# Optimization experiments

Hardware: AMD Instinct MI355X
Metric: run time of the kernel (lower is better)

The kernel has to match this reference:

```python
import jax, jax.numpy as jnp
import numpy as np

NEG_SLOPE = 0.2   # PyG GATConv default negative_slope
LN_EPS = 1e-5
SOFTMAX_EPS = 1e-16  # PyG softmax denominator eps


def setup_inputs() -> dict:
    key = jax.random.key(0)
    ks = jax.random.split(key, 6)
    N, IN, OUT, H, E = 100000, 128, 64, 2, 1600000
    X = jax.random.normal(ks[0], (N, IN), dtype=jnp.float32)
    edge_index = jax.random.randint(ks[1], (2, E), 0, N, dtype=jnp.int64)
    W = jax.random.normal(ks[2], (H * OUT, IN), dtype=jnp.float32) * 0.05
    att_src = jax.random.normal(ks[3], (H, OUT), dtype=jnp.float32) * 0.05
    att_dst = jax.random.normal(ks[4], (H, OUT), dtype=jnp.float32) * 0.05
    bias = jnp.zeros((OUT,), dtype=jnp.float32)
    ln_gamma = jnp.ones((OUT,), dtype=jnp.float32)
    ln_beta = jnp.zeros((OUT,), dtype=jnp.float32)
    return {"X": X, "edge_index": edge_index, "W": W, "att_src": att_src,
            "att_dst": att_dst, "bias": bias, "ln_gamma": ln_gamma, "ln_beta": ln_beta}


def reference(X, edge_index, W, att_src, att_dst, bias, ln_gamma, ln_beta):
    N = X.shape[0]
    H, F = att_src.shape
    # PyG GATConv default: add self-loops
    loops = jnp.arange(N, dtype=edge_index.dtype)
    src = jnp.concatenate([edge_index[0], loops])  # [Et]
    dst = jnp.concatenate([edge_index[1], loops])  # [Et]
    # linear projection: x' = X @ W^T  -> [N, H, F]
    x = (X @ W.T).reshape(N, H, F)
    # per-node attention logits  [N, H]
    a_src = jnp.einsum('nhf,hf->nh', x, att_src)
    a_dst = jnp.einsum('nhf,hf->nh', x, att_dst)
    # per-edge logits, leaky relu  [Et, H]
    e = jax.nn.leaky_relu(a_src[src] + a_dst[dst], NEG_SLOPE)
    # segment softmax over incoming edges of each dst node
    m = jax.ops.segment_max(e, dst, num_segments=N)          # [N, H]
    ex = jnp.exp(e - m[dst])
    denom = jax.ops.segment_sum(ex, dst, num_segments=N)     # [N, H]
    alpha = ex / (denom[dst] + SOFTMAX_EPS)                  # [Et, H]
    # weighted scatter-add of source features
    msg = x[src] * alpha[:, :, None]                         # [Et, H, F]
    out = jax.ops.segment_sum(msg, dst, num_segments=N)      # [N, H, F]
    # concat=False -> mean over heads, then bias
    out = out.mean(axis=1) + bias                            # [N, F]
    # LayerNorm over features
    mu = out.mean(axis=-1, keepdims=True)
    var = ((out - mu) ** 2).mean(axis=-1, keepdims=True)
    h = (out - mu) * jax.lax.rsqrt(var + LN_EPS) * ln_gamma + ln_beta
    return h
```

## Files before the change

### kernel.cpp

```cpp
#include <hip/hip_runtime.h>
#include <hip/hip_bf16.h>

#define NEG_SLOPE 0.2f
#define LN_EPS 1e-5f
#define SM_EPS 1e-16f

typedef __attribute__((ext_vector_type(8))) short bf16x8;
typedef __attribute__((ext_vector_type(4))) float f32x4;

__device__ inline unsigned short f2bf(float f) {
    unsigned u = __float_as_uint(f);
    return (unsigned short)((u + 0x7FFFu + ((u >> 16) & 1u)) >> 16);
}
__device__ inline float bf_lo(unsigned int v) { return __uint_as_float(v << 16); }
__device__ inline float bf_hi(unsigned int v) { return __uint_as_float(v & 0xffff0000u); }

#define NBIN 512
#define BCAP 4864
#define SCHUNK 2048
#define CURPAD 16

__global__ __launch_bounds__(256) void k_gemm(const float* __restrict__ X,
                                              const float* __restrict__ W,
                                              const float* __restrict__ att_src,
                                              const float* __restrict__ att_dst,
                                              unsigned int* __restrict__ xp,
                                              float2* __restrict__ aS,
                                              float2* __restrict__ aD,
                                              int* __restrict__ binCursor, int N) {
    __shared__ unsigned short Ws[128 * 136];
    __shared__ unsigned short Xs[64 * 136];
    const int t = threadIdx.x;
    const int b0 = blockIdx.x * 64;
    const int lane = t & 63;
    const int w = t >> 6;
    const int c15 = lane & 15;
    const int quad = lane >> 4;

    if (blockIdx.x == 0) {
        for (int i = t; i < NBIN; i += 256) binCursor[i * CURPAD] = i * BCAP;
    }

#pragma unroll
    for (int i = 0; i < 16; ++i) {
        int f = i * 256 + t;
        int nr = f >> 5;
        int q = f & 31;
        float4 v = reinterpret_cast<const float4*>(W)[nr * 32 + q];
        ushort4 b;
        b.x = f2bf(v.x); b.y = f2bf(v.y); b.z = f2bf(v.z); b.w = f2bf(v.w);
        *reinterpret_cast<ushort4*>(&Ws[nr * 136 + q * 4]) = b;
    }
#pragma unroll
    for (int i = 0; i < 8; ++i) {
        int f = i * 256 + t;
        int m = f >> 5;
        int q = f & 31;
        int gr = b0 + m;
        if (gr >= N) gr = N - 1;
        float4 v = reinterpret_cast<const float4*>(X)[(size_t)gr * 32 + q];
        ushort4 b;
        b.x = f2bf(v.x); b.y = f2bf(v.y); b.z = f2bf(v.z); b.w = f2bf(v.w);
        *reinterpret_cast<ushort4*>(&Xs[m * 136 + q * 4]) = b;
    }
    __syncthreads();

    f32x4 acc[8];
#pragma unroll
    for (int ct = 0; ct < 8; ++ct) acc[ct] = (f32x4){0.f, 0.f, 0.f, 0.f};

#pragma unroll
    for (int kc = 0; kc < 4; ++kc) {
        bf16x8 af = *reinterpret_cast<const bf16x8*>(
            &Xs[(w * 16 + c15) * 136 + kc * 32 + quad * 8]);
#pragma unroll
        for (int ct = 0; ct < 8; ++ct) {
            bf16x8 bfr = *reinterpret_cast<const bf16x8*>(
                &Ws[(ct * 16 + c15) * 136 + kc * 32 + quad * 8]);
            acc[ct] = __builtin_amdgcn_mfma_f32_16x16x32_bf16(af, bfr, acc[ct], 0, 0, 0);
        }
    }

    float attS[8], attD[8];
#pragma unroll
    for (int ct = 0; ct < 8; ++ct) {
        attS[ct] = att_src[ct * 16 + c15];
        attD[ct] = att_dst[ct * 16 + c15];
    }

#pragma unroll
    for (int r = 0; r < 4; ++r) {
        int row = b0 + w * 16 + quad * 4 + r;
        float s0 = 0.f, s1 = 0.f, d0 = 0.f, d1 = 0.f;
#pragma unroll
        for (int ct = 0; ct < 4; ++ct) {
            s0 += acc[ct][r] * attS[ct];
            d0 += acc[ct][r] * attD[ct];
            s1 += acc[ct + 4][r] * attS[ct + 4];
            d1 += acc[ct + 4][r] * attD[ct + 4];
        }
#pragma unroll
        for (int o = 1; o < 16; o <<= 1) {
            s0 += __shfl_xor(s0, o);
            s1 += __shfl_xor(s1, o);
            d0 += __shfl_xor(d0, o);
            d1 += __shfl_xor(d1, o);
        }
        if (row < N) {
#pragma unroll
            for (int ct = 0; ct < 4; ++ct) {
                unsigned int p = (unsigned int)f2bf(acc[ct][r]) |
                                 ((unsigned int)f2bf(acc[ct + 4][r]) << 16);
                xp[(size_t)row * 64 + ct * 16 + c15] = p;
            }
            if (c15 == 0) {
                aS[row] = make_float2(s0, s1);
                aD[row] = make_float2(d0, d1);
            }
        }
    }
}

__global__ __launch_bounds__(256) void k_scatter(const int* __restrict__ ei,
                                                 const float2* __restrict__ aS,
                                                 const float2* __restrict__ aD,
                                                 int* __restrict__ binCursor,
                                                 uint2* __restrict__ tmp, int E) {
    __shared__ int off[NBIN];
    const int t = threadIdx.x;
    const int base = blockIdx.x * SCHUNK;

    int se[8], de[8];
    unsigned int ue[8];
#pragma unroll
    for (int k = 0; k < 8; ++k) {
        int i = base + k * 256 + t;
        if (i < E) {
            int s = ei[i];
            int d = ei[E + i];
            se[k] = s; de[k] = d;
            float2 a = aS[s];
            float2 ad2 = aD[d];
            float f0 = a.x + ad2.x; f0 = fmaxf(f0, NEG_SLOPE * f0);
            float f1 = a.y + ad2.y; f1 = fmaxf(f1, NEG_SLOPE * f1);
            ue[k] = (unsigned int)f2bf(__expf(f0)) |
                    ((unsigned int)f2bf(__expf(f1)) << 16);
        } else {
            de[k] = -1;
        }
    }

    for (int i = t; i < NBIN; i += 256) off[i] = 0;
    __syncthreads();
#pragma unroll
    for (int k = 0; k < 8; ++k)
        if (de[k] >= 0) atomicAdd(&off[de[k] >> 8], 1);
    __syncthreads();
    for (int i = t; i < NBIN; i += 256) {
        int h = off[i];
        off[i] = h ? atomicAdd(&binCursor[i * CURPAD], h) : 0;
    }
    __syncthreads();
#pragma unroll
    for (int k = 0; k < 8; ++k) {
        if (de[k] >= 0) {
            int p = atomicAdd(&off[de[k] >> 8], 1);
            tmp[p] = make_uint2(((unsigned)(de[k] & 255) << 24) | (unsigned)se[k],
                                ue[k]);
        }
    }
}

__global__ __launch_bounds__(512) void k_bucket(const uint2* __restrict__ tmp,
                                                const int* __restrict__ binCursor,
                                                uint2* __restrict__ csr,
                                                unsigned int* __restrict__ rowPtr,
                                                int N) {
    __shared__ int cnt[256];
    __shared__ int cur[256];
    __shared__ int lds[4];
    const int t = threadIdx.x;
    const int b = blockIdx.x;
    const int start = b * BCAP;
    int m = binCursor[b * CURPAD] - start;
    if (m > BCAP) m = BCAP;

    if (t < 256) cnt[t] = 0;
    __syncthreads();

    for (int k = t; k < m; k += 512) {
        uint2 e = tmp[start + k];
        atomicAdd(&cnt[e.x >> 24], 1);
    }
    __syncthreads();

    const int lane = t & 63, w = t >> 6;
    int v = 0, incl = 0;
    if (t < 256) {
        v = cnt[t];
        incl = v;
#pragma unroll
        for (int o = 1; o < 64; o <<= 1) {
            int u = __shfl_up(incl, o);
            if (lane >= o) incl += u;
        }
        if (lane == 63) lds[w] = incl;
    }
    __syncthreads();
    if (t == 0) {
        int run = 0;
        for (int i = 0; i < 4; ++i) { int tv = lds[i]; lds[i] = run; run += tv; }
    }
    __syncthreads();
    if (t < 256) {
        int excl = lds[w] + incl - v;
        cur[t] = excl;
        int d = b * 256 + t;
        if (d < N) rowPtr[d] = (unsigned)(start + excl) | ((unsigned)v << 22);
    }
    __syncthreads();

    for (int k = t; k < m; k += 512) {
        uint2 e = tmp[start + k];
        int li = e.x >> 24;
        int p = atomicAdd(&cur[li], 1);
        csr[start + p] = make_uint2(e.x & 0x00FFFFFFu, e.y);
    }
}

__global__ __launch_bounds__(256) void k_agg(const unsigned int* __restrict__ xp,
                                             const float2* __restrict__ aS,
                                             const float2* __restrict__ aD,
                                             const unsigned int* __restrict__ rowPtr,
                                             const uint2* __restrict__ csr,
                                             const float* __restrict__ bias,
                                             const float* __restrict__ gamma,
                                             const float* __restrict__ beta,
                                             float* __restrict__ out, int N) {
    const int w = threadIdx.x >> 6, lane = threadIdx.x & 63;
    const int n = blockIdx.x * 4 + w;
    if (n >= N) return;

    float2 a = aS[n];
    float2 ad2 = aD[n];
    float f0 = a.x + ad2.x; f0 = fmaxf(f0, NEG_SLOPE * f0);
    float f1 = a.y + ad2.y; f1 = fmaxf(f1, NEG_SLOPE * f1);
    float us0 = __expf(f0), us1 = __expf(f1);

    unsigned int vself = xp[(size_t)n * 64 + lane];
    float S0 = us0 * bf_lo(vself);
    float S1 = us1 * bf_hi(vself);
    float D0 = us0, D1 = us1;

    unsigned int pr = rowPtr[n];
    const int jb = (int)(pr & 0x3FFFFFu);
    const int je = jb + (int)(pr >> 22);
    int j = jb;
    const int nfull = (je - jb) >> 3;

    uint2 cc[8];
    if (nfull > 0) {
        int ju = __builtin_amdgcn_readfirstlane(j);
#pragma unroll
        for (int q = 0; q < 8; ++q) cc[q] = csr[ju + q];
    }
    for (int bI = 0; bI < nfull; ++bI) {
        unsigned int v[8];
#pragma unroll
        for (int q = 0; q < 8; ++q) v[q] = xp[(size_t)cc[q].x * 64 + lane];
        uint2 cn[8];
        {
            int jn = (bI + 1 < nfull) ? (j + 8) : jb;
            int ju = __builtin_amdgcn_readfirstlane(jn);
#pragma unroll
            for (int q = 0; q < 8; ++q) cn[q] = csr[ju + q];
        }
#pragma unroll
        for (int q = 0; q < 8; ++q) {
            float u0 = bf_lo(cc[q].y), u1 = bf_hi(cc[q].y);
            D0 += u0; D1 += u1;
            S0 += u0 * bf_lo(v[q]);
            S1 += u1 * bf_hi(v[q]);
        }
#pragma unroll
        for (int q = 0; q < 8; ++q) cc[q] = cn[q];
        j += 8;
    }
    for (; j + 3 < je; j += 4) {
        int ju = __builtin_amdgcn_readfirstlane(j);
        uint2 c[4];
#pragma unroll
        for (int q = 0; q < 4; ++q) c[q] = csr[ju + q];
        unsigned int v[4];
#pragma unroll
        for (int q = 0; q < 4; ++q) v[q] = xp[(size_t)c[q].x * 64 + lane];
#pragma unroll
        for (int q = 0; q < 4; ++q) {
            float u0 = bf_lo(c[q].y), u1 = bf_hi(c[q].y);
            D0 += u0; D1 += u1;
            S0 += u0 * bf_lo(v[q]);
            S1 += u1 * bf_hi(v[q]);
        }
    }
    for (; j < je; ++j) {
        uint2 c = csr[__builtin_amdgcn_readfirstlane(j)];
        unsigned int vv = xp[(size_t)c.x * 64 + lane];
        float u0 = bf_lo(c.y), u1 = bf_hi(c.y);
        D0 += u0; D1 += u1;
        S0 += u0 * bf_lo(vv);
        S1 += u1 * bf_hi(vv);
    }

    float o = (0.5f / (D0 + SM_EPS)) * S0 + (0.5f / (D1 + SM_EPS)) * S1 + bias[lane];

    float mu = o;
#pragma unroll
    for (int d = 32; d > 0; d >>= 1) mu += __shfl_xor(mu, d);
    mu *= (1.0f / 64.0f);
    float dv = o - mu;
    float var = dv * dv;
#pragma unroll
    for (int d = 32; d > 0; d >>= 1) var += __shfl_xor(var, d);
    var *= (1.0f / 64.0f);
    out[(size_t)n * 64 + lane] = dv * rsqrtf(var + LN_EPS) * gamma[lane] + beta[lane];
}

extern "C" void kernel_launch(void* const* d_in, const int* in_sizes, int n_in,
                              void* d_out, int out_size, void* d_ws, size_t ws_size,
                              hipStream_t stream) {
    const float* X        = (const float*)d_in[0];
    const int*   ei       = (const int*)d_in[1];
    const float* W        = (const float*)d_in[2];
    const float* att_src  = (const float*)d_in[3];
    const float* att_dst  = (const float*)d_in[4];
    const float* bias     = (const float*)d_in[5];
    const float* ln_gamma = (const float*)d_in[6];
    const float* ln_beta  = (const float*)d_in[7];
    float* out = (float*)d_out;

    const int N = in_sizes[0] / 128;
    const int E = in_sizes[1] / 2;
    const int NBUCK = (N + 255) / 256;

    char* ws = (char*)d_ws;
    size_t off = 0;
    auto alloc = [&](size_t bytes) {
        size_t o = off;
        off += (bytes + 255) & ~(size_t)255;
        return o;
    };
    unsigned int* xp     = (unsigned int*)(ws + alloc((size_t)N * 64 * 4));
    float2* aS           = (float2*)(ws + alloc((size_t)N * 8));
    float2* aD           = (float2*)(ws + alloc((size_t)N * 8));
    unsigned int* rowPtr = (unsigned int*)(ws + alloc((size_t)N * 4));
    uint2* csr           = (uint2*)(ws + alloc((size_t)NBIN * BCAP * 8));
    uint2* tmp           = (uint2*)(ws + alloc((size_t)NBIN * BCAP * 8));
    int* binCursor       = (int*)(ws + alloc(NBIN * CURPAD * 4));

    k_gemm<<<(N + 63) / 64, 256, 0, stream>>>(X, W, att_src, att_dst, xp, aS, aD,
                                              binCursor, N);
    k_scatter<<<(E + SCHUNK - 1) / SCHUNK, 256, 0, stream>>>(ei, aS, aD,
                                                             binCursor, tmp, E);
    k_bucket<<<NBUCK, 512, 0, stream>>>(tmp, binCursor, csr, rowPtr, N);
    k_agg<<<(N + 3) / 4, 256, 0, stream>>>(xp, aS, aD, rowPtr, csr,
                                           bias, ln_gamma, ln_beta, out, N);
}
```

Measured before the change: 237.1 us.

## Recompute edge attention weights in aggregation and shrink CSR entries to 4 bytes

The scatter kernel no longer gathers aS/aD or computes exp per edge. It only writes a packed 4-byte (local dst, src) word, which halves the tmp and csr traffic in the scatter, bucket and aggregation kernels. The aggregation kernel now gathers aS[src] per edge and recomputes leaky-relu and exp in fp32 inline. This adds a random 8-byte gather and two exps per edge inside the aggregation loop. The scatter chunk size is also doubled to 16 edges per thread, and the index math switches to 32-bit shifts.

```diff
diff --git a/kernel.cpp b/kernel.cpp
--- a/kernel.cpp
+++ b/kernel.cpp
@@ -17,7 +17,7 @@
 
 #define NBIN 512
 #define BCAP 4864
-#define SCHUNK 2048
+#define SCHUNK 4096
 #define CURPAD 16
 
 __global__ __launch_bounds__(256) void k_gemm(const float* __restrict__ X,
@@ -122,39 +122,33 @@
 }
 
 __global__ __launch_bounds__(256) void k_scatter(const int* __restrict__ ei,
-                                                 const float2* __restrict__ aS,
-                                                 const float2* __restrict__ aD,
                                                  int* __restrict__ binCursor,
-                                                 uint2* __restrict__ tmp, int E) {
+                                                 unsigned int* __restrict__ tmp,
+                                                 int E) {
     __shared__ int off[NBIN];
     const int t = threadIdx.x;
     const int base = blockIdx.x * SCHUNK;
 
-    int se[8], de[8];
-    unsigned int ue[8];
-#pragma unroll
-    for (int k = 0; k < 8; ++k) {
+    int bn[16];
+    unsigned int pe[16];
+#pragma unroll
+    for (int k = 0; k < 16; ++k) {
         int i = base + k * 256 + t;
         if (i < E) {
             int s = ei[i];
             int d = ei[E + i];
-            se[k] = s; de[k] = d;
-            float2 a = aS[s];
-            float2 ad2 = aD[d];
-            float f0 = a.x + ad2.x; f0 = fmaxf(f0, NEG_SLOPE * f0);
-            float f1 = a.y + ad2.y; f1 = fmaxf(f1, NEG_SLOPE * f1);
-            ue[k] = (unsigned int)f2bf(__expf(f0)) |
-                    ((unsigned int)f2bf(__expf(f1)) << 16);
+            bn[k] = d >> 8;
+            pe[k] = ((unsigned)(d & 255) << 24) | (unsigned)s;
         } else {
-            de[k] = -1;
+            bn[k] = -1;
         }
     }
 
     for (int i = t; i < NBIN; i += 256) off[i] = 0;
     __syncthreads();
 #pragma unroll
-    for (int k = 0; k < 8; ++k)
-        if (de[k] >= 0) atomicAdd(&off[de[k] >> 8], 1);
+    for (int k = 0; k < 16; ++k)
+        if (bn[k] >= 0) atomicAdd(&off[bn[k]], 1);
     __syncthreads();
     for (int i = t; i < NBIN; i += 256) {
         int h = off[i];
@@ -162,18 +156,17 @@
     }
     __syncthreads();
 #pragma unroll
-    for (int k = 0; k < 8; ++k) {
-        if (de[k] >= 0) {
-            int p = atomicAdd(&off[de[k] >> 8], 1);
-            tmp[p] = make_uint2(((unsigned)(de[k] & 255) << 24) | (unsigned)se[k],
-                                ue[k]);
-        }
-    }
-}
-
-__global__ __launch_bounds__(512) void k_bucket(const uint2* __restrict__ tmp,
+    for (int k = 0; k < 16; ++k) {
+        if (bn[k] >= 0) {
+            int p = atomicAdd(&off[bn[k]], 1);
+            tmp[p] = pe[k];
+        }
+    }
+}
+
+__global__ __launch_bounds__(512) void k_bucket(const unsigned int* __restrict__ tmp,
                                                 const int* __restrict__ binCursor,
-                                                uint2* __restrict__ csr,
+                                                unsigned int* __restrict__ csr,
                                                 unsigned int* __restrict__ rowPtr,
                                                 int N) {
     __shared__ int cnt[256];
@@ -189,8 +182,7 @@
     __syncthreads();
 
     for (int k = t; k < m; k += 512) {
-        uint2 e = tmp[start + k];
-        atomicAdd(&cnt[e.x >> 24], 1);
+        atomicAdd(&cnt[tmp[start + k] >> 24], 1);
     }
     __syncthreads();
 
@@ -221,10 +213,9 @@
     __syncthreads();
 
     for (int k = t; k < m; k += 512) {
-        uint2 e = tmp[start + k];
-        int li = e.x >> 24;
-        int p = atomicAdd(&cur[li], 1);
-        csr[start + p] = make_uint2(e.x & 0x00FFFFFFu, e.y);
+        unsigned int e = tmp[start + k];
+        int p = atomicAdd(&cur[e >> 24], 1);
+        csr[start + p] = e & 0x00FFFFFFu;
     }
 }
 
@@ -232,7 +223,7 @@
                                              const float2* __restrict__ aS,
                                              const float2* __restrict__ aD,
                                              const unsigned int* __restrict__ rowPtr,
-                                             const uint2* __restrict__ csr,
+                                             const unsigned int* __restrict__ csr,
                                              const float* __restrict__ bias,
                                              const float* __restrict__ gamma,
                                              const float* __restrict__ beta,
@@ -247,7 +238,7 @@
     float f1 = a.y + ad2.y; f1 = fmaxf(f1, NEG_SLOPE * f1);
     float us0 = __expf(f0), us1 = __expf(f1);
 
-    unsigned int vself = xp[(size_t)n * 64 + lane];
+    unsigned int vself = xp[((unsigned)n << 6) | lane];
     float S0 = us0 * bf_lo(vself);
     float S1 = us1 * bf_hi(vself);
     float D0 = us0, D1 = us1;
@@ -258,7 +249,7 @@
     int j = jb;
     const int nfull = (je - jb) >> 3;
 
-    uint2 cc[8];
+    unsigned int cc[8];
     if (nfull > 0) {
         int ju = __builtin_amdgcn_readfirstlane(j);
 #pragma unroll
@@ -266,9 +257,12 @@
     }
     for (int bI = 0; bI < nfull; ++bI) {
         unsigned int v[8];
-#pragma unroll
-        for (int q = 0; q < 8; ++q) v[q] = xp[(size_t)cc[q].x * 64 + lane];
-        uint2 cn[8];
+        float2 as_[8];
+#pragma unroll
+        for (int q = 0; q < 8; ++q) v[q] = xp[(cc[q] << 6) | lane];
+#pragma unroll
+        for (int q = 0; q < 8; ++q) as_[q] = aS[cc[q]];
+        unsigned int cn[8];
         {
             int jn = (bI + 1 < nfull) ? (j + 8) : jb;
             int ju = __builtin_amdgcn_readfirstlane(jn);
@@ -277,7 +271,9 @@
         }
 #pragma unroll
         for (int q = 0; q < 8; ++q) {
-            float u0 = bf_lo(cc[q].y), u1 = bf_hi(cc[q].y);
+            float g0 = as_[q].x + ad2.x; g0 = fmaxf(g0, NEG_SLOPE * g0);
+            float g1 = as_[q].y + ad2.y; g1 = fmaxf(g1, NEG_SLOPE * g1);
+            float u0 = __expf(g0), u1 = __expf(g1);
             D0 += u0; D1 += u1;
             S0 += u0 * bf_lo(v[q]);
             S1 += u1 * bf_hi(v[q]);
@@ -288,24 +284,32 @@
     }
     for (; j + 3 < je; j += 4) {
         int ju = __builtin_amdgcn_readfirstlane(j);
-        uint2 c[4];
+        unsigned int c[4];
 #pragma unroll
         for (int q = 0; q < 4; ++q) c[q] = csr[ju + q];
         unsigned int v[4];
-#pragma unroll
-        for (int q = 0; q < 4; ++q) v[q] = xp[(size_t)c[q].x * 64 + lane];
+        float2 as_[4];
+#pragma unroll
+        for (int q = 0; q < 4; ++q) v[q] = xp[(c[q] << 6) | lane];
+#pragma unroll
+        for (int q = 0; q < 4; ++q) as_[q] = aS[c[q]];
 #pragma unroll
         for (int q = 0; q < 4; ++q) {
-            float u0 = bf_lo(c[q].y), u1 = bf_hi(c[q].y);
+            float g0 = as_[q].x + ad2.x; g0 = fmaxf(g0, NEG_SLOPE * g0);
+            float g1 = as_[q].y + ad2.y; g1 = fmaxf(g1, NEG_SLOPE * g1);
+            float u0 = __expf(g0), u1 = __expf(g1);
             D0 += u0; D1 += u1;
             S0 += u0 * bf_lo(v[q]);
             S1 += u1 * bf_hi(v[q]);
         }
     }
     for (; j < je; ++j) {
-        uint2 c = csr[__builtin_amdgcn_readfirstlane(j)];
-        unsigned int vv = xp[(size_t)c.x * 64 + lane];
-        float u0 = bf_lo(c.y), u1 = bf_hi(c.y);
+        unsigned int c = csr[__builtin_amdgcn_readfirstlane(j)];
+        unsigned int vv = xp[(c << 6) | lane];
+        float2 asv = aS[c];
+        float g0 = asv.x + ad2.x; g0 = fmaxf(g0, NEG_SLOPE * g0);
+        float g1 = asv.y + ad2.y; g1 = fmaxf(g1, NEG_SLOPE * g1);
+        float u0 = __expf(g0), u1 = __expf(g1);
         D0 += u0; D1 += u1;
         S0 += u0 * bf_lo(vv);
         S1 += u1 * bf_hi(vv);
@@ -353,14 +357,13 @@
     float2* aS           = (float2*)(ws + alloc((size_t)N * 8));
     float2* aD           = (float2*)(ws + alloc((size_t)N * 8));
     unsigned int* rowPtr = (unsigned int*)(ws + alloc((size_t)N * 4));
-    uint2* csr           = (uint2*)(ws + alloc((size_t)NBIN * BCAP * 8));
-    uint2* tmp           = (uint2*)(ws + alloc((size_t)NBIN * BCAP * 8));
+    unsigned int* csr    = (unsigned int*)(ws + alloc((size_t)NBIN * BCAP * 4));
+    unsigned int* tmp    = (unsigned int*)(ws + alloc((size_t)NBIN * BCAP * 4));
     int* binCursor       = (int*)(ws + alloc(NBIN * CURPAD * 4));
 
     k_gemm<<<(N + 63) / 64, 256, 0, stream>>>(X, W, att_src, att_dst, xp, aS, aD,
                                               binCursor, N);
-    k_scatter<<<(E + SCHUNK - 1) / SCHUNK, 256, 0, stream>>>(ei, aS, aD,
-                                                             binCursor, tmp, E);
+    k_scatter<<<(E + SCHUNK - 1) / SCHUNK, 256, 0, stream>>>(ei, binCursor, tmp, E);
     k_bucket<<<NBUCK, 512, 0, stream>>>(tmp, binCursor, csr, rowPtr, N);
     k_agg<<<(N + 3) / 4, 256, 0, stream>>>(xp, aS, aD, rowPtr, csr,
                                            bias, ln_gamma, ln_beta, out, N);
```

New measurement: 231.2 us. 1.03x faster.
